# Performance work log

Hardware: AMD Instinct MI355X
Metric: run time of the kernel (lower is better)

## Reference

```python
import jax, jax.numpy as jnp
import numpy as np
from jax import lax

B, C, H, W = 8, 64, 128, 128
KS = 3          # kernel size
K = KS * KS     # kernel field = 9
PAD = 1


def conv2d(x, w, b):
    # x: [B,Cin,H,W], w: [Cout,Cin,kh,kw], 'same' 3x3 conv
    y = lax.conv_general_dilated(x, w, window_strides=(1, 1),
                                 padding=((PAD, PAD), (PAD, PAD)),
                                 dimension_numbers=('NCHW', 'OIHW', 'NCHW'))
    return y + b[None, :, None, None]


def modulated_deform_conv(x, offset, mask, weight, bias):
    # x:[B,C,H,W], offset:[B,2K,H,W] (dy,dx per tap), mask:[B,K,H,W]
    Bs, Cin, Hin, Win = x.shape
    off = offset.reshape(Bs, K, 2, Hin, Win)
    ky, kx = jnp.meshgrid(jnp.arange(KS), jnp.arange(KS), indexing='ij')
    ky = ky.reshape(K).astype(x.dtype)   # kernel tap row offsets 0..2
    kx = kx.reshape(K).astype(x.dtype)
    # sampling positions p = p0 + p_k + offset (stride=1, pad=1)
    py = (jnp.arange(Hin, dtype=x.dtype)[None, None, :, None] - PAD
          + ky[None, :, None, None] + off[:, :, 0])            # [B,K,H,W]
    px = (jnp.arange(Win, dtype=x.dtype)[None, None, None, :] - PAD
          + kx[None, :, None, None] + off[:, :, 1])            # [B,K,H,W]

    y0 = jnp.floor(py); x0 = jnp.floor(px)
    ly = py - y0; lx = px - x0                                  # frac parts
    y0i = y0.astype(jnp.int32); x0i = x0.astype(jnp.int32)

    x_flat = x.reshape(Bs, Cin, Hin * Win)

    def gather(iy, ix):
        valid = ((iy >= 0) & (iy < Hin) & (ix >= 0) & (ix < Win))
        flat = (jnp.clip(iy, 0, Hin - 1) * Win + jnp.clip(ix, 0, Win - 1))
        g = jax.vmap(lambda xb, ib: xb[:, ib])(x_flat, flat.reshape(Bs, -1))
        g = g.reshape(Bs, Cin, K, Hin, Win)
        return g * valid[:, None].astype(x.dtype)

    w00 = ((1 - ly) * (1 - lx))[:, None]  # [B,1,K,H,W]
    w01 = ((1 - ly) * lx)[:, None]
    w10 = (ly * (1 - lx))[:, None]
    w11 = (ly * lx)[:, None]

    val = (w00 * gather(y0i, x0i) + w01 * gather(y0i, x0i + 1)
           + w10 * gather(y0i + 1, x0i) + w11 * gather(y0i + 1, x0i + 1))
    val = val * mask[:, None]                                   # modulation
    out = jnp.einsum('ock,bckhw->bohw', weight.reshape(weight.shape[0], Cin, K), val)
    return out + bias[None, :, None, None]


def setup_inputs() -> dict:
    key = jax.random.key(0)
    ks = jax.random.split(key, 7)
    s = 0.05
    return {
        'x': jax.random.normal(ks[0], (B, C, H, W), jnp.float32),
        'w_om': jax.random.normal(ks[1], (3 * K, C, KS, KS), jnp.float32) * s,
        'b_om': jax.random.normal(ks[2], (3 * K,), jnp.float32) * s,
        'w_dc': jax.random.normal(ks[3], (C, C, KS, KS), jnp.float32) * s,
        'b_dc': jax.random.normal(ks[4], (C,), jnp.float32) * s,
        'w_c': jax.random.normal(ks[5], (C, C, KS, KS), jnp.float32) * s,
        'b_c': jax.random.normal(ks[6], (C,), jnp.float32) * s,
    }


def reference(x, w_om, b_om, w_dc, b_dc, w_c, b_c):
    om = conv2d(x, w_om, b_om)                       # [B,3K,H,W]
    offset, mask_raw = om[:, :2 * K], om[:, 2 * K:]
    mask = 2.0 * jax.nn.sigmoid(mask_raw)
    out = modulated_deform_conv(x, offset, mask, w_dc, b_dc)
    act = jnp.where(out > 0, out, 0.2 * out)         # LeakyReLU(0.2)
    return conv2d(act, w_c, b_c) + x
```

## Files before the change

### kernel.cpp

```cpp
#include <hip/hip_runtime.h>
#include <math.h>

#define Bn 8
#define Cn 64
#define Hn 128
#define Wn 128
#define HWn (Hn * Wn)
#define Kn 9

#define XSW 40
#define XSROW (66 * XSW)
#define XSCC (3 * XSROW)

typedef __attribute__((ext_vector_type(8))) short short8;
typedef __attribute__((ext_vector_type(4))) float floatx4;

__device__ __forceinline__ float bf2f(short s) {
  return __uint_as_float(((unsigned)(unsigned short)s) << 16);
}
__device__ __forceinline__ short f2bf(float f) {
  unsigned u = __float_as_uint(f);
  u += 0x7fff + ((u >> 16) & 1);
  return (short)(u >> 16);
}

__global__ __launch_bounds__(256) void k_prep_w(
    const float* __restrict__ w_om, const float* __restrict__ w_dc,
    const float* __restrict__ w_c, short* __restrict__ wt) {
  int idx = blockIdx.x * 256 + threadIdx.x;
  if (idx >= 160 * 576) return;
  int row = idx / 576, k = idx - row * 576;
  int kk = k >> 6, cin = k & 63;
  float v;
  if (row < 32)
    v = (row < 27) ? w_om[(row * 64 + cin) * 9 + kk] : 0.f;
  else if (row < 96)
    v = w_dc[((row - 32) * 64 + cin) * 9 + kk];
  else
    v = w_c[((row - 96) * 64 + cin) * 9 + kk];
  wt[idx] = f2bf(v);
}

__global__ __launch_bounds__(256) void k_prep_x(const float* __restrict__ x,
                                                short* __restrict__ xT2) {
  __shared__ float tile[64][129];
  const int h = blockIdx.x, b = blockIdx.y;
  const int tid = threadIdx.x;
  const float* xb = x + (size_t)b * 64 * HWn + h * Wn;
  for (int i = tid; i < 8192; i += 256) {
    int c = i >> 7, w = i & 127;
    tile[c][w] = xb[c * HWn + w];
  }
  __syncthreads();
  for (int i = tid; i < 2048; i += 256) {
    int w = i >> 4, c4 = (i & 15) * 4;
    int half = c4 >> 5, cl = c4 & 31;
    short4 o;
    o.x = f2bf(tile[c4 + 0][w]);
    o.y = f2bf(tile[c4 + 1][w]);
    o.z = f2bf(tile[c4 + 2][w]);
    o.w = f2bf(tile[c4 + 3][w]);
    *(short4*)(xT2 + ((size_t)(b * 2 + half) * HWn + h * Wn + w) * 32 + cl) = o;
  }
}

__global__ __launch_bounds__(256, 4) void k_omdef(
    const short* __restrict__ xT2, const short* __restrict__ wt,
    const float* __restrict__ b_om, const float* __restrict__ b_dc,
    short* __restrict__ actT2) {
  __shared__ __attribute__((aligned(16))) char raw[64 * 296 * 2];
  short* xs = (short*)raw;
  float* som = (float*)(raw + XSCC * 2);
  short(*val)[296] = (short(*)[296])raw;

  const int b = blockIdx.z, h = blockIdx.y, w0 = blockIdx.x * 64;
  const int tid = threadIdx.x;
  const int wave = tid >> 6, lane = tid & 63, quad = lane >> 4, lr = lane & 15;
  const short* xb2 = xT2 + (size_t)b * 2 * HWn * 32;

  floatx4 zf = {0.f, 0.f, 0.f, 0.f};
  floatx4 aco0 = zf, aco1 = zf;
  const int mo0 = (wave & 1) * 16;
  const int n0 = (wave >> 1) * 32;

  for (int cc = 0; cc < 2; ++cc) {
    if (cc) __syncthreads();
    for (int j = tid; j < 792; j += 256) {
      int c8 = (j & 3) * 8;
      int r = j >> 2;
      int ky = r / 66, p = r - ky * 66;
      int gy = h + ky - 1, gx = w0 - 1 + p;
      short8 v = {0, 0, 0, 0, 0, 0, 0, 0};
      if (gy >= 0 && gy < Hn && gx >= 0 && gx < Wn)
        v = *(const short8*)(xb2 + ((size_t)cc * HWn + gy * Wn + gx) * 32 + c8);
      *(short8*)(xs + ky * XSROW + p * XSW + c8) = v;
    }
    __syncthreads();
    const short* wbo = wt + cc * 32 + quad * 8;
#pragma unroll
    for (int kk = 0; kk < 9; ++kk) {
      int ky = kk / 3, kx = kk - ky * 3;
      short8 a = *(const short8*)(wbo + (mo0 + lr) * 576 + kk * 64);
      const short* bp = xs + ky * XSROW + kx * XSW + quad * 8;
      short8 b0 = *(const short8*)(bp + (n0 + lr) * XSW);
      short8 b1 = *(const short8*)(bp + (n0 + 16 + lr) * XSW);
      aco0 = __builtin_amdgcn_mfma_f32_16x16x32_bf16(a, b0, aco0, 0, 0, 0);
      aco1 = __builtin_amdgcn_mfma_f32_16x16x32_bf16(a, b1, aco1, 0, 0, 0);
    }
  }
#pragma unroll
  for (int nt = 0; nt < 2; ++nt) {
    floatx4 a = nt ? aco1 : aco0;
    int px = n0 + nt * 16 + lr;
#pragma unroll
    for (int r = 0; r < 4; ++r) {
      int co = mo0 + quad * 4 + r;
      if (co < 27) {
        float v = a[r] + b_om[co];
        if (co >= 18) v = 2.f / (1.f + expf(-v));
        som[co * 65 + px] = v;
      }
    }
  }
  __syncthreads();

  unsigned pa01[3], pa23[3], pu01[3], pu23[3];
#pragma unroll
  for (int t = 0; t < 3; ++t) {
    int pr = tid + t * 256;
    if (pr < 576) {
      int k = pr >> 6, p = pr & 63;
      float offy = som[(2 * k) * 65 + p];
      float offx = som[(2 * k + 1) * 65 + p];
      float m = som[(18 + k) * 65 + p];
      float py = (float)(h - 1 + (k / 3)) + offy;
      float px_ = (float)(w0 + p - 1 + (k % 3)) + offx;
      float fy = floorf(py), fx = floorf(px_);
      float ly = py - fy, lx = px_ - fx;
      int iy0 = (int)fy, ix0 = (int)fx;
      int iy1 = iy0 + 1, ix1 = ix0 + 1;
      bool vy0 = (iy0 >= 0) && (iy0 < Hn);
      bool vy1 = (iy1 >= 0) && (iy1 < Hn);
      bool vx0 = (ix0 >= 0) && (ix0 < Wn);
      bool vx1 = (ix1 >= 0) && (ix1 < Wn);
      unsigned cy0 = (unsigned)min(max(iy0, 0), Hn - 1);
      unsigned cy1 = (unsigned)min(max(iy1, 0), Hn - 1);
      unsigned cx0 = (unsigned)min(max(ix0, 0), Wn - 1);
      unsigned cx1 = (unsigned)min(max(ix1, 0), Wn - 1);
      pa01[t] = (cy0 * Wn + cx0) | ((cy0 * Wn + cx1) << 16);
      pa23[t] = (cy1 * Wn + cx0) | ((cy1 * Wn + cx1) << 16);
      float u0 = (vy0 && vx0) ? (1.f - ly) * (1.f - lx) * m : 0.f;
      float u1 = (vy0 && vx1) ? (1.f - ly) * lx * m : 0.f;
      float u2 = (vy1 && vx0) ? ly * (1.f - lx) * m : 0.f;
      float u3 = (vy1 && vx1) ? ly * lx * m : 0.f;
      pu01[t] = (unsigned)(unsigned short)f2bf(u0) |
                ((unsigned)(unsigned short)f2bf(u1) << 16);
      pu23[t] = (unsigned)(unsigned short)f2bf(u2) |
                ((unsigned)(unsigned short)f2bf(u3) << 16);
    }
  }
  __syncthreads();

  floatx4 acc[2][2] = {{zf, zf}, {zf, zf}};
  const int m0 = (wave & 1) * 32;

  for (int cc = 0; cc < 2; ++cc) {
    if (cc) __syncthreads();
#pragma unroll
    for (int t = 0; t < 3; ++t) {
      int pr = tid + t * 256;
      if (pr < 576) {
        int k = pr >> 6, p = pr & 63;
        int a0 = pa01[t] & 0xFFFF, a1 = pa01[t] >> 16;
        int a2 = pa23[t] & 0xFFFF, a3 = pa23[t] >> 16;
        float u0 = bf2f((short)(pu01[t] & 0xFFFF));
        float u1 = bf2f((short)(pu01[t] >> 16));
        float u2 = bf2f((short)(pu23[t] & 0xFFFF));
        float u3 = bf2f((short)(pu23[t] >> 16));
        const short* s0 = xb2 + ((size_t)cc * HWn + a0) * 32;
        const short* s1 = xb2 + ((size_t)cc * HWn + a1) * 32;
        const short* s2 = xb2 + ((size_t)cc * HWn + a2) * 32;
        const short* s3 = xb2 + ((size_t)cc * HWn + a3) * 32;
#pragma unroll
        for (int c8 = 0; c8 < 32; c8 += 8) {
          short8 q0 = *(const short8*)(s0 + c8);
          short8 q1 = *(const short8*)(s1 + c8);
          short8 q2 = *(const short8*)(s2 + c8);
          short8 q3 = *(const short8*)(s3 + c8);
          short8 o;
#pragma unroll
          for (int e = 0; e < 8; ++e) {
            float f = u0 * bf2f(q0[e]) + u1 * bf2f(q1[e]) +
                      u2 * bf2f(q2[e]) + u3 * bf2f(q3[e]);
            o[e] = f2bf(f);
          }
          *(short8*)&val[p][k * 32 + c8] = o;
        }
      }
    }
    __syncthreads();
    const short* wbd = wt + 32 * 576 + cc * 32 + quad * 8;
#pragma unroll
    for (int kk = 0; kk < 9; ++kk) {
      short8 a0 = *(const short8*)(wbd + (m0 + lr) * 576 + kk * 64);
      short8 a1 = *(const short8*)(wbd + (m0 + 16 + lr) * 576 + kk * 64);
      short8 b0 = *(const short8*)&val[n0 + lr][kk * 32 + quad * 8];
      short8 b1 = *(const short8*)&val[n0 + 16 + lr][kk * 32 + quad * 8];
      acc[0][0] = __builtin_amdgcn_mfma_f32_16x16x32_bf16(a0, b0, acc[0][0], 0, 0, 0);
      acc[0][1] = __builtin_amdgcn_mfma_f32_16x16x32_bf16(a0, b1, acc[0][1], 0, 0, 0);
      acc[1][0] = __builtin_amdgcn_mfma_f32_16x16x32_bf16(a1, b0, acc[1][0], 0, 0, 0);
      acc[1][1] = __builtin_amdgcn_mfma_f32_16x16x32_bf16(a1, b1, acc[1][1], 0, 0, 0);
    }
  }

#pragma unroll
  for (int mt = 0; mt < 2; ++mt) {
#pragma unroll
    for (int nt = 0; nt < 2; ++nt) {
      int px = n0 + nt * 16 + lr;
      int c0 = m0 + mt * 16 + quad * 4;
      int half = c0 >> 5, cl = c0 & 31;
      short4 o;
      float v;
      v = acc[mt][nt][0] + b_dc[c0 + 0]; o.x = f2bf(v > 0.f ? v : 0.2f * v);
      v = acc[mt][nt][1] + b_dc[c0 + 1]; o.y = f2bf(v > 0.f ? v : 0.2f * v);
      v = acc[mt][nt][2] + b_dc[c0 + 2]; o.z = f2bf(v > 0.f ? v : 0.2f * v);
      v = acc[mt][nt][3] + b_dc[c0 + 3]; o.w = f2bf(v > 0.f ? v : 0.2f * v);
      *(short4*)(actT2 +
                 ((size_t)(b * 2 + half) * HWn + h * Wn + w0 + px) * 32 + cl) = o;
    }
  }
}

__global__ __launch_bounds__(256, 5) void k_conv_out(
    const short* __restrict__ actT2, const short* __restrict__ wt,
    const float* __restrict__ b_c, const float* __restrict__ x,
    float* __restrict__ out) {
  __shared__ __attribute__((aligned(16))) short as_[2 * XSCC];

  const int b = blockIdx.z, h = blockIdx.y, w0 = blockIdx.x * 64;
  const int tid = threadIdx.x;
  const int wave = tid >> 6, lane = tid & 63, quad = lane >> 4, lr = lane & 15;
  const short* ab2 = actT2 + (size_t)b * 2 * HWn * 32;

  for (int j = tid; j < 1584; j += 256) {
    int cc = j / 792, r = j - cc * 792;
    int c8 = (r & 3) * 8;
    int r2 = r >> 2;
    int ky = r2 / 66, p = r2 - ky * 66;
    int gy = h + ky - 1, gx = w0 - 1 + p;
    short8 v = {0, 0, 0, 0, 0, 0, 0, 0};
    if (gy >= 0 && gy < Hn && gx >= 0 && gx < Wn)
      v = *(const short8*)(ab2 + ((size_t)cc * HWn + gy * Wn + gx) * 32 + c8);
    *(short8*)(as_ + cc * XSCC + ky * XSROW + p * XSW + c8) = v;
  }
  __syncthreads();

  floatx4 zf = {0.f, 0.f, 0.f, 0.f};
  floatx4 acc[2][2] = {{zf, zf}, {zf, zf}};
  const int m0 = (wave & 1) * 32;
  const int n0 = (wave >> 1) * 32;

  for (int cc = 0; cc < 2; ++cc) {
    const short* wbc = wt + 96 * 576 + cc * 32 + quad * 8;
#pragma unroll
    for (int kk = 0; kk < 9; ++kk) {
      int ky = kk / 3, kx = kk - ky * 3;
      short8 a0 = *(const short8*)(wbc + (m0 + lr) * 576 + kk * 64);
      short8 a1 = *(const short8*)(wbc + (m0 + 16 + lr) * 576 + kk * 64);
      const short* bp = as_ + cc * XSCC + ky * XSROW + kx * XSW + quad * 8;
      short8 b0 = *(const short8*)(bp + (n0 + lr) * XSW);
      short8 b1 = *(const short8*)(bp + (n0 + 16 + lr) * XSW);
      acc[0][0] = __builtin_amdgcn_mfma_f32_16x16x32_bf16(a0, b0, acc[0][0], 0, 0, 0);
      acc[0][1] = __builtin_amdgcn_mfma_f32_16x16x32_bf16(a0, b1, acc[0][1], 0, 0, 0);
      acc[1][0] = __builtin_amdgcn_mfma_f32_16x16x32_bf16(a1, b0, acc[1][0], 0, 0, 0);
      acc[1][1] = __builtin_amdgcn_mfma_f32_16x16x32_bf16(a1, b1, acc[1][1], 0, 0, 0);
    }
  }

#pragma unroll
  for (int mt = 0; mt < 2; ++mt) {
#pragma unroll
    for (int nt = 0; nt < 2; ++nt) {
      int px = n0 + nt * 16 + lr;
#pragma unroll
      for (int r = 0; r < 4; ++r) {
        int cout = m0 + mt * 16 + quad * 4 + r;
        size_t gidx = ((size_t)(b * 64 + cout) * Hn + h) * Wn + w0 + px;
        out[gidx] = acc[mt][nt][r] + b_c[cout] + x[gidx];
      }
    }
  }
}

extern "C" void kernel_launch(void* const* d_in, const int* in_sizes, int n_in,
                              void* d_out, int out_size, void* d_ws,
                              size_t ws_size, hipStream_t stream) {
  const float* x = (const float*)d_in[0];
  const float* w_om = (const float*)d_in[1];
  const float* b_om = (const float*)d_in[2];
  const float* w_dc = (const float*)d_in[3];
  const float* b_dc = (const float*)d_in[4];
  const float* w_c = (const float*)d_in[5];
  const float* b_c = (const float*)d_in[6];
  float* out = (float*)d_out;

  short* xT2 = (short*)d_ws;
  short* actT2 = xT2 + (size_t)Bn * 2 * HWn * 32;
  short* wt = actT2 + (size_t)Bn * 2 * HWn * 32;

  k_prep_w<<<dim3((160 * 576 + 255) / 256), 256, 0, stream>>>(w_om, w_dc, w_c, wt);
  k_prep_x<<<dim3(Hn, Bn), 256, 0, stream>>>(x, xT2);
  k_omdef<<<dim3(2, Hn, Bn), 256, 0, stream>>>(xT2, wt, b_om, b_dc, actT2);
  k_conv_out<<<dim3(2, Hn, Bn), 256, 0, stream>>>(actT2, wt, b_c, x, out);
}
```

Measured before the change: 261.2 us.

## Switch to NHWC 64-channel layout, MFMA-fragment weight packing, LDS sampling tables

Activations and x now use a single NHWC bf16 layout with all 64 channels per pixel instead of two 32-channel halves. Weights are pre-packed in MFMA fragment order so each lane reads a contiguous 16 bytes. Bilinear sample indices and weights move from registers into shared memory, and the gather loop is redistributed so each thread handles one 8-channel chunk. Other changes: LDS row padding shrinks (XSW 40→36, VSTRIDE 292), the grid is flattened with batch as the fastest index so neighbouring blocks hit different images, and k_omdef occupancy drops to 3. The aim is better gather coalescing, fewer VGPRs and better L2 locality, at the cost of more LDS and possible bank conflicts.

```diff
diff --git a/kernel.cpp b/kernel.cpp
--- a/kernel.cpp
+++ b/kernel.cpp
@@ -8,9 +8,14 @@
 #define HWn (Hn * Wn)
 #define Kn 9
 
-#define XSW 40
+#define XSW 36
 #define XSROW (66 * XSW)
 #define XSCC (3 * XSROW)
+#define VSTRIDE 292
+
+#define WOM_OFF 0
+#define WDC_OFF 18432
+#define WC_OFF 55296
 
 typedef __attribute__((ext_vector_type(8))) short short8;
 typedef __attribute__((ext_vector_type(4))) float floatx4;
@@ -28,23 +33,32 @@
     const float* __restrict__ w_om, const float* __restrict__ w_dc,
     const float* __restrict__ w_c, short* __restrict__ wt) {
   int idx = blockIdx.x * 256 + threadIdx.x;
-  if (idx >= 160 * 576) return;
-  int row = idx / 576, k = idx - row * 576;
-  int kk = k >> 6, cin = k & 63;
+  if (idx >= 92160) return;
   float v;
-  if (row < 32)
+  if (idx < WDC_OFF) {
+    int e = idx;
+    int elem = e & 7, lane = (e >> 3) & 63, mt = (e >> 9) & 1, t = e >> 10;
+    int kk = t % 9, cc = t / 9;
+    int row = mt * 16 + (lane & 15);
+    int cin = cc * 32 + (lane >> 4) * 8 + elem;
     v = (row < 27) ? w_om[(row * 64 + cin) * 9 + kk] : 0.f;
-  else if (row < 96)
-    v = w_dc[((row - 32) * 64 + cin) * 9 + kk];
-  else
-    v = w_c[((row - 96) * 64 + cin) * 9 + kk];
+  } else {
+    int e = (idx < WC_OFF) ? idx - WDC_OFF : idx - WC_OFF;
+    const float* src = (idx < WC_OFF) ? w_dc : w_c;
+    int elem = e & 7, lane = (e >> 3) & 63, mt = (e >> 9) & 3, t = e >> 11;
+    int kk = t % 9, cc = t / 9;
+    int row = mt * 16 + (lane & 15);
+    int cin = cc * 32 + (lane >> 4) * 8 + elem;
+    v = src[(row * 64 + cin) * 9 + kk];
+  }
   wt[idx] = f2bf(v);
 }
 
 __global__ __launch_bounds__(256) void k_prep_x(const float* __restrict__ x,
-                                                short* __restrict__ xT2) {
+                                                short* __restrict__ xT) {
   __shared__ float tile[64][129];
-  const int h = blockIdx.x, b = blockIdx.y;
+  const int bid = blockIdx.x;
+  const int b = bid & 7, h = bid >> 3;
   const int tid = threadIdx.x;
   const float* xb = x + (size_t)b * 64 * HWn + h * Wn;
   for (int i = tid; i < 8192; i += 256) {
@@ -52,55 +66,61 @@
     tile[c][w] = xb[c * HWn + w];
   }
   __syncthreads();
+  short* dst = xT + ((size_t)(b * Hn + h) * Wn) * 64;
   for (int i = tid; i < 2048; i += 256) {
     int w = i >> 4, c4 = (i & 15) * 4;
-    int half = c4 >> 5, cl = c4 & 31;
     short4 o;
     o.x = f2bf(tile[c4 + 0][w]);
     o.y = f2bf(tile[c4 + 1][w]);
     o.z = f2bf(tile[c4 + 2][w]);
     o.w = f2bf(tile[c4 + 3][w]);
-    *(short4*)(xT2 + ((size_t)(b * 2 + half) * HWn + h * Wn + w) * 32 + cl) = o;
-  }
-}
-
-__global__ __launch_bounds__(256, 4) void k_omdef(
-    const short* __restrict__ xT2, const short* __restrict__ wt,
+    *(short4*)(dst + (size_t)w * 64 + c4) = o;
+  }
+}
+
+__global__ __launch_bounds__(256, 3) void k_omdef(
+    const short* __restrict__ xT, const short* __restrict__ wt,
     const float* __restrict__ b_om, const float* __restrict__ b_dc,
-    short* __restrict__ actT2) {
-  __shared__ __attribute__((aligned(16))) char raw[64 * 296 * 2];
+    short* __restrict__ actT) {
+  __shared__ __attribute__((aligned(16))) char raw[64 * VSTRIDE * 2 + 9216];
   short* xs = (short*)raw;
   float* som = (float*)(raw + XSCC * 2);
-  short(*val)[296] = (short(*)[296])raw;
-
-  const int b = blockIdx.z, h = blockIdx.y, w0 = blockIdx.x * 64;
+  short(*val)[VSTRIDE] = (short(*)[VSTRIDE])raw;
+  unsigned* sbw = (unsigned*)(raw + 64 * VSTRIDE * 2);
+  unsigned* sb01 = sbw, *sb23 = sbw + 576, *sw01 = sbw + 1152,
+          *sw23 = sbw + 1728;
+
+  const int bid = blockIdx.x;
+  const int b = bid & 7;
+  const int r = bid >> 3;
+  const int h = r >> 1, w0 = (r & 1) * 64;
   const int tid = threadIdx.x;
   const int wave = tid >> 6, lane = tid & 63, quad = lane >> 4, lr = lane & 15;
-  const short* xb2 = xT2 + (size_t)b * 2 * HWn * 32;
+  const short* xb = xT + (size_t)b * HWn * 64;
 
   floatx4 zf = {0.f, 0.f, 0.f, 0.f};
   floatx4 aco0 = zf, aco1 = zf;
-  const int mo0 = (wave & 1) * 16;
+  const int mto = wave & 1;
   const int n0 = (wave >> 1) * 32;
 
   for (int cc = 0; cc < 2; ++cc) {
     if (cc) __syncthreads();
     for (int j = tid; j < 792; j += 256) {
       int c8 = (j & 3) * 8;
-      int r = j >> 2;
-      int ky = r / 66, p = r - ky * 66;
+      int rr = j >> 2;
+      int ky = rr / 66, p = rr - ky * 66;
       int gy = h + ky - 1, gx = w0 - 1 + p;
       short8 v = {0, 0, 0, 0, 0, 0, 0, 0};
       if (gy >= 0 && gy < Hn && gx >= 0 && gx < Wn)
-        v = *(const short8*)(xb2 + ((size_t)cc * HWn + gy * Wn + gx) * 32 + c8);
+        v = *(const short8*)(xb + (size_t)(gy * Wn + gx) * 64 + cc * 32 + c8);
       *(short8*)(xs + ky * XSROW + p * XSW + c8) = v;
     }
     __syncthreads();
-    const short* wbo = wt + cc * 32 + quad * 8;
 #pragma unroll
     for (int kk = 0; kk < 9; ++kk) {
       int ky = kk / 3, kx = kk - ky * 3;
-      short8 a = *(const short8*)(wbo + (mo0 + lr) * 576 + kk * 64);
+      short8 a = *(const short8*)(wt + WOM_OFF +
+                                  (((cc * 9 + kk) * 2 + mto) * 64 + lane) * 8);
       const short* bp = xs + ky * XSROW + kx * XSW + quad * 8;
       short8 b0 = *(const short8*)(bp + (n0 + lr) * XSW);
       short8 b1 = *(const short8*)(bp + (n0 + 16 + lr) * XSW);
@@ -113,10 +133,10 @@
     floatx4 a = nt ? aco1 : aco0;
     int px = n0 + nt * 16 + lr;
 #pragma unroll
-    for (int r = 0; r < 4; ++r) {
-      int co = mo0 + quad * 4 + r;
+    for (int rr = 0; rr < 4; ++rr) {
+      int co = mto * 16 + quad * 4 + rr;
       if (co < 27) {
-        float v = a[r] + b_om[co];
+        float v = a[rr] + b_om[co];
         if (co >= 18) v = 2.f / (1.f + expf(-v));
         som[co * 65 + px] = v;
       }
@@ -124,86 +144,73 @@
   }
   __syncthreads();
 
-  unsigned pa01[3], pa23[3], pu01[3], pu23[3];
-#pragma unroll
-  for (int t = 0; t < 3; ++t) {
-    int pr = tid + t * 256;
-    if (pr < 576) {
-      int k = pr >> 6, p = pr & 63;
-      float offy = som[(2 * k) * 65 + p];
-      float offx = som[(2 * k + 1) * 65 + p];
-      float m = som[(18 + k) * 65 + p];
-      float py = (float)(h - 1 + (k / 3)) + offy;
-      float px_ = (float)(w0 + p - 1 + (k % 3)) + offx;
-      float fy = floorf(py), fx = floorf(px_);
-      float ly = py - fy, lx = px_ - fx;
-      int iy0 = (int)fy, ix0 = (int)fx;
-      int iy1 = iy0 + 1, ix1 = ix0 + 1;
-      bool vy0 = (iy0 >= 0) && (iy0 < Hn);
-      bool vy1 = (iy1 >= 0) && (iy1 < Hn);
-      bool vx0 = (ix0 >= 0) && (ix0 < Wn);
-      bool vx1 = (ix1 >= 0) && (ix1 < Wn);
-      unsigned cy0 = (unsigned)min(max(iy0, 0), Hn - 1);
-      unsigned cy1 = (unsigned)min(max(iy1, 0), Hn - 1);
-      unsigned cx0 = (unsigned)min(max(ix0, 0), Wn - 1);
-      unsigned cx1 = (unsigned)min(max(ix1, 0), Wn - 1);
-      pa01[t] = (cy0 * Wn + cx0) | ((cy0 * Wn + cx1) << 16);
-      pa23[t] = (cy1 * Wn + cx0) | ((cy1 * Wn + cx1) << 16);
-      float u0 = (vy0 && vx0) ? (1.f - ly) * (1.f - lx) * m : 0.f;
-      float u1 = (vy0 && vx1) ? (1.f - ly) * lx * m : 0.f;
-      float u2 = (vy1 && vx0) ? ly * (1.f - lx) * m : 0.f;
-      float u3 = (vy1 && vx1) ? ly * lx * m : 0.f;
-      pu01[t] = (unsigned)(unsigned short)f2bf(u0) |
-                ((unsigned)(unsigned short)f2bf(u1) << 16);
-      pu23[t] = (unsigned)(unsigned short)f2bf(u2) |
-                ((unsigned)(unsigned short)f2bf(u3) << 16);
-    }
+  for (int pr = tid; pr < 576; pr += 256) {
+    int k = pr >> 6, p = pr & 63;
+    float offy = som[(2 * k) * 65 + p];
+    float offx = som[(2 * k + 1) * 65 + p];
+    float m = som[(18 + k) * 65 + p];
+    float py = (float)(h - 1 + (k / 3)) + offy;
+    float px_ = (float)(w0 + p - 1 + (k % 3)) + offx;
+    float fy = floorf(py), fx = floorf(px_);
+    float ly = py - fy, lx = px_ - fx;
+    int iy0 = (int)fy, ix0 = (int)fx;
+    int iy1 = iy0 + 1, ix1 = ix0 + 1;
+    bool vy0 = (iy0 >= 0) && (iy0 < Hn);
+    bool vy1 = (iy1 >= 0) && (iy1 < Hn);
+    bool vx0 = (ix0 >= 0) && (ix0 < Wn);
+    bool vx1 = (ix1 >= 0) && (ix1 < Wn);
+    unsigned cy0 = (unsigned)min(max(iy0, 0), Hn - 1);
+    unsigned cy1 = (unsigned)min(max(iy1, 0), Hn - 1);
+    unsigned cx0 = (unsigned)min(max(ix0, 0), Wn - 1);
+    unsigned cx1 = (unsigned)min(max(ix1, 0), Wn - 1);
+    sb01[pr] = (cy0 * Wn + cx0) | ((cy0 * Wn + cx1) << 16);
+    sb23[pr] = (cy1 * Wn + cx0) | ((cy1 * Wn + cx1) << 16);
+    float u0 = (vy0 && vx0) ? (1.f - ly) * (1.f - lx) * m : 0.f;
+    float u1 = (vy0 && vx1) ? (1.f - ly) * lx * m : 0.f;
+    float u2 = (vy1 && vx0) ? ly * (1.f - lx) * m : 0.f;
+    float u3 = (vy1 && vx1) ? ly * lx * m : 0.f;
+    sw01[pr] = (unsigned)(unsigned short)f2bf(u0) |
+               ((unsigned)(unsigned short)f2bf(u1) << 16);
+    sw23[pr] = (unsigned)(unsigned short)f2bf(u2) |
+               ((unsigned)(unsigned short)f2bf(u3) << 16);
   }
   __syncthreads();
 
   floatx4 acc[2][2] = {{zf, zf}, {zf, zf}};
-  const int m0 = (wave & 1) * 32;
+  const int mt0 = (wave & 1) * 2;
 
   for (int cc = 0; cc < 2; ++cc) {
     if (cc) __syncthreads();
-#pragma unroll
-    for (int t = 0; t < 3; ++t) {
-      int pr = tid + t * 256;
-      if (pr < 576) {
-        int k = pr >> 6, p = pr & 63;
-        int a0 = pa01[t] & 0xFFFF, a1 = pa01[t] >> 16;
-        int a2 = pa23[t] & 0xFFFF, a3 = pa23[t] >> 16;
-        float u0 = bf2f((short)(pu01[t] & 0xFFFF));
-        float u1 = bf2f((short)(pu01[t] >> 16));
-        float u2 = bf2f((short)(pu23[t] & 0xFFFF));
-        float u3 = bf2f((short)(pu23[t] >> 16));
-        const short* s0 = xb2 + ((size_t)cc * HWn + a0) * 32;
-        const short* s1 = xb2 + ((size_t)cc * HWn + a1) * 32;
-        const short* s2 = xb2 + ((size_t)cc * HWn + a2) * 32;
-        const short* s3 = xb2 + ((size_t)cc * HWn + a3) * 32;
-#pragma unroll
-        for (int c8 = 0; c8 < 32; c8 += 8) {
-          short8 q0 = *(const short8*)(s0 + c8);
-          short8 q1 = *(const short8*)(s1 + c8);
-          short8 q2 = *(const short8*)(s2 + c8);
-          short8 q3 = *(const short8*)(s3 + c8);
-          short8 o;
-#pragma unroll
-          for (int e = 0; e < 8; ++e) {
-            float f = u0 * bf2f(q0[e]) + u1 * bf2f(q1[e]) +
-                      u2 * bf2f(q2[e]) + u3 * bf2f(q3[e]);
-            o[e] = f2bf(f);
-          }
-          *(short8*)&val[p][k * 32 + c8] = o;
-        }
+    for (int j = tid; j < 2304; j += 256) {
+      int chunk = j & 3, pr = j >> 2;
+      int p = pr & 63, k = pr >> 6;
+      unsigned a01 = sb01[pr], a23 = sb23[pr];
+      unsigned uw01 = sw01[pr], uw23 = sw23[pr];
+      float u0 = bf2f((short)(uw01 & 0xFFFF));
+      float u1 = bf2f((short)(uw01 >> 16));
+      float u2 = bf2f((short)(uw23 & 0xFFFF));
+      float u3 = bf2f((short)(uw23 >> 16));
+      int co = cc * 32 + chunk * 8;
+      short8 q0 = *(const short8*)(xb + (size_t)(a01 & 0xFFFF) * 64 + co);
+      short8 q1 = *(const short8*)(xb + (size_t)(a01 >> 16) * 64 + co);
+      short8 q2 = *(const short8*)(xb + (size_t)(a23 & 0xFFFF) * 64 + co);
+      short8 q3 = *(const short8*)(xb + (size_t)(a23 >> 16) * 64 + co);
+      short8 o;
+#pragma unroll
+      for (int e = 0; e < 8; ++e) {
+        float f = u0 * bf2f(q0[e]) + u1 * bf2f(q1[e]) + u2 * bf2f(q2[e]) +
+                  u3 * bf2f(q3[e]);
+        o[e] = f2bf(f);
       }
+      *(short8*)&val[p][k * 32 + chunk * 8] = o;
     }
     __syncthreads();
-    const short* wbd = wt + 32 * 576 + cc * 32 + quad * 8;
 #pragma unroll
     for (int kk = 0; kk < 9; ++kk) {
-      short8 a0 = *(const short8*)(wbd + (m0 + lr) * 576 + kk * 64);
-      short8 a1 = *(const short8*)(wbd + (m0 + 16 + lr) * 576 + kk * 64);
+      short8 a0 = *(const short8*)(wt + WDC_OFF +
+                                   (((cc * 9 + kk) * 4 + mt0) * 64 + lane) * 8);
+      short8 a1 = *(const short8*)(wt + WDC_OFF +
+                                   (((cc * 9 + kk) * 4 + mt0 + 1) * 64 + lane) * 8);
       short8 b0 = *(const short8*)&val[n0 + lr][kk * 32 + quad * 8];
       short8 b1 = *(const short8*)&val[n0 + 16 + lr][kk * 32 + quad * 8];
       acc[0][0] = __builtin_amdgcn_mfma_f32_16x16x32_bf16(a0, b0, acc[0][0], 0, 0, 0);
@@ -213,61 +220,64 @@
     }
   }
 
+  short* ab = actT + ((size_t)(b * Hn + h) * Wn + w0) * 64;
 #pragma unroll
   for (int mt = 0; mt < 2; ++mt) {
 #pragma unroll
     for (int nt = 0; nt < 2; ++nt) {
       int px = n0 + nt * 16 + lr;
-      int c0 = m0 + mt * 16 + quad * 4;
-      int half = c0 >> 5, cl = c0 & 31;
+      int c0 = (mt0 + mt) * 16 + quad * 4;
       short4 o;
       float v;
       v = acc[mt][nt][0] + b_dc[c0 + 0]; o.x = f2bf(v > 0.f ? v : 0.2f * v);
       v = acc[mt][nt][1] + b_dc[c0 + 1]; o.y = f2bf(v > 0.f ? v : 0.2f * v);
       v = acc[mt][nt][2] + b_dc[c0 + 2]; o.z = f2bf(v > 0.f ? v : 0.2f * v);
       v = acc[mt][nt][3] + b_dc[c0 + 3]; o.w = f2bf(v > 0.f ? v : 0.2f * v);
-      *(short4*)(actT2 +
-                 ((size_t)(b * 2 + half) * HWn + h * Wn + w0 + px) * 32 + cl) = o;
+      *(short4*)(ab + (size_t)px * 64 + c0) = o;
     }
   }
 }
 
 __global__ __launch_bounds__(256, 5) void k_conv_out(
-    const short* __restrict__ actT2, const short* __restrict__ wt,
+    const short* __restrict__ actT, const short* __restrict__ wt,
     const float* __restrict__ b_c, const float* __restrict__ x,
     float* __restrict__ out) {
   __shared__ __attribute__((aligned(16))) short as_[2 * XSCC];
 
-  const int b = blockIdx.z, h = blockIdx.y, w0 = blockIdx.x * 64;
+  const int bid = blockIdx.x;
+  const int b = bid & 7;
+  const int r = bid >> 3;
+  const int h = r >> 1, w0 = (r & 1) * 64;
   const int tid = threadIdx.x;
   const int wave = tid >> 6, lane = tid & 63, quad = lane >> 4, lr = lane & 15;
-  const short* ab2 = actT2 + (size_t)b * 2 * HWn * 32;
+  const short* ab = actT + (size_t)b * HWn * 64;
 
   for (int j = tid; j < 1584; j += 256) {
-    int cc = j / 792, r = j - cc * 792;
-    int c8 = (r & 3) * 8;
-    int r2 = r >> 2;
+    int cc = j / 792, rr = j - cc * 792;
+    int c8 = (rr & 3) * 8;
+    int r2 = rr >> 2;
     int ky = r2 / 66, p = r2 - ky * 66;
     int gy = h + ky - 1, gx = w0 - 1 + p;
     short8 v = {0, 0, 0, 0, 0, 0, 0, 0};
     if (gy >= 0 && gy < Hn && gx >= 0 && gx < Wn)
-      v = *(const short8*)(ab2 + ((size_t)cc * HWn + gy * Wn + gx) * 32 + c8);
+      v = *(const short8*)(ab + (size_t)(gy * Wn + gx) * 64 + cc * 32 + c8);
     *(short8*)(as_ + cc * XSCC + ky * XSROW + p * XSW + c8) = v;
   }
   __syncthreads();
 
   floatx4 zf = {0.f, 0.f, 0.f, 0.f};
   floatx4 acc[2][2] = {{zf, zf}, {zf, zf}};
-  const int m0 = (wave & 1) * 32;
+  const int mt0 = (wave & 1) * 2;
   const int n0 = (wave >> 1) * 32;
 
   for (int cc = 0; cc < 2; ++cc) {
-    const short* wbc = wt + 96 * 576 + cc * 32 + quad * 8;
 #pragma unroll
     for (int kk = 0; kk < 9; ++kk) {
       int ky = kk / 3, kx = kk - ky * 3;
-      short8 a0 = *(const short8*)(wbc + (m0 + lr) * 576 + kk * 64);
-      short8 a1 = *(const short8*)(wbc + (m0 + 16 + lr) * 576 + kk * 64);
+      short8 a0 = *(const short8*)(wt + WC_OFF +
+                                   (((cc * 9 + kk) * 4 + mt0) * 64 + lane) * 8);
+      short8 a1 = *(const short8*)(wt + WC_OFF +
+                                   (((cc * 9 + kk) * 4 + mt0 + 1) * 64 + lane) * 8);
       const short* bp = as_ + cc * XSCC + ky * XSROW + kx * XSW + quad * 8;
       short8 b0 = *(const short8*)(bp + (n0 + lr) * XSW);
       short8 b1 = *(const short8*)(bp + (n0 + 16 + lr) * XSW);
@@ -284,10 +294,10 @@
     for (int nt = 0; nt < 2; ++nt) {
       int px = n0 + nt * 16 + lr;
 #pragma unroll
-      for (int r = 0; r < 4; ++r) {
-        int cout = m0 + mt * 16 + quad * 4 + r;
+      for (int rr = 0; rr < 4; ++rr) {
+        int cout = (mt0 + mt) * 16 + quad * 4 + rr;
         size_t gidx = ((size_t)(b * 64 + cout) * Hn + h) * Wn + w0 + px;
-        out[gidx] = acc[mt][nt][r] + b_c[cout] + x[gidx];
+        out[gidx] = acc[mt][nt][rr] + b_c[cout] + x[gidx];
       }
     }
   }
@@ -305,12 +315,12 @@
   const float* b_c = (const float*)d_in[6];
   float* out = (float*)d_out;
 
-  short* xT2 = (short*)d_ws;
-  short* actT2 = xT2 + (size_t)Bn * 2 * HWn * 32;
-  short* wt = actT2 + (size_t)Bn * 2 * HWn * 32;
-
-  k_prep_w<<<dim3((160 * 576 + 255) / 256), 256, 0, stream>>>(w_om, w_dc, w_c, wt);
-  k_prep_x<<<dim3(Hn, Bn), 256, 0, stream>>>(x, xT2);
-  k_omdef<<<dim3(2, Hn, Bn), 256, 0, stream>>>(xT2, wt, b_om, b_dc, actT2);
-  k_conv_out<<<dim3(2, Hn, Bn), 256, 0, stream>>>(actT2, wt, b_c, x, out);
-}
+  short* xT = (short*)d_ws;
+  short* actT = xT + (size_t)Bn * HWn * 64;
+  short* wt = actT + (size_t)Bn * HWn * 64;
+
+  k_prep_w<<<dim3(360), 256, 0, stream>>>(w_om, w_dc, w_c, wt);
+  k_prep_x<<<dim3(1024), 256, 0, stream>>>(x, xT);
+  k_omdef<<<dim3(2048), 256, 0, stream>>>(xT, wt, b_om, b_dc, actT);
+  k_conv_out<<<dim3(2048), 256, 0, stream>>>(actT, wt, b_c, x, out);
+}
```

New measurement: 237.5 us. 9.1% less time.
